# Kernel optimization log

Measured on AMD Instinct MI355X. Metric: run time of the kernel, lower is better.

Reference implementation:

```python
import jax, jax.numpy as jnp
import numpy as np

D_MODEL = 1024
D_STATE = 16
D_CONV = 4
EXPAND = 2
D_INNER = EXPAND * D_MODEL          # 2048
DT_RANK = (D_MODEL + 15) // 16      # 64
B, L = 4, 2048


def setup_inputs() -> dict:
    key = jax.random.key(0)
    ks = jax.random.split(key, 10)
    s = 0.02
    x = jax.random.normal(ks[0], (B, L, D_MODEL), dtype=jnp.float32)
    # weights stored (in, out) so y = x @ W
    W_in = jax.random.normal(ks[1], (D_MODEL, 2 * D_INNER), dtype=jnp.float32) * s
    conv_w = jax.random.normal(ks[2], (D_INNER, D_CONV), dtype=jnp.float32) * 0.2
    conv_b = jnp.zeros((D_INNER,), dtype=jnp.float32)
    W_xproj = jax.random.normal(ks[3], (D_INNER, DT_RANK + 2 * D_STATE), dtype=jnp.float32) * s
    W_dt = jax.random.normal(ks[4], (DT_RANK, D_INNER), dtype=jnp.float32) * s
    b_dt = jax.random.uniform(ks[5], (D_INNER,), dtype=jnp.float32, minval=-4.0, maxval=-2.0)
    # S4D real init: A = -exp(A_log), A_log = log(1..d_state)
    A_log = jnp.log(jnp.broadcast_to(jnp.arange(1, D_STATE + 1, dtype=jnp.float32), (D_INNER, D_STATE)))
    Dp = jnp.ones((D_INNER,), dtype=jnp.float32)
    W_out = jax.random.normal(ks[6], (D_INNER, D_MODEL), dtype=jnp.float32) * s
    return {"x": x, "W_in": W_in, "conv_w": conv_w, "conv_b": conv_b,
            "W_xproj": W_xproj, "W_dt": W_dt, "b_dt": b_dt,
            "A_log": A_log, "Dp": Dp, "W_out": W_out}


def _causal_depthwise_conv(u, conv_w, conv_b):
    # u: (B, L, D_INNER); depthwise causal conv, kernel D_CONV
    uc = jnp.transpose(u, (0, 2, 1))                      # (B, D, L)
    k = conv_w[:, None, :]                                # (D, 1, K)
    y = jax.lax.conv_general_dilated(
        uc, k, window_strides=(1,), padding=[(D_CONV - 1, 0)],
        feature_group_count=D_INNER,
        dimension_numbers=('NCH', 'OIH', 'NCH'))
    y = y + conv_b[None, :, None]
    return jnp.transpose(y, (0, 2, 1))                    # (B, L, D)


def _selective_scan(u, delta, A, Bm, Cm, Dp):
    # u, delta: (B, L, d); A: (d, n); Bm, Cm: (B, L, n)
    def step(h, inp):
        u_t, dt_t, B_t, C_t = inp                         # (B,d),(B,d),(B,n),(B,n)
        dA = jnp.exp(dt_t[..., None] * A)                 # (B, d, n)
        h = h * dA + (dt_t * u_t)[..., None] * B_t[:, None, :]
        y = jnp.einsum('bdn,bn->bd', h, C_t)
        return h, y

    h0 = jnp.zeros((u.shape[0], u.shape[2], A.shape[1]), dtype=u.dtype)
    xs = (jnp.swapaxes(u, 0, 1), jnp.swapaxes(delta, 0, 1),
          jnp.swapaxes(Bm, 0, 1), jnp.swapaxes(Cm, 0, 1))
    _, ys = jax.lax.scan(step, h0, xs)
    y = jnp.swapaxes(ys, 0, 1)                            # (B, L, d)
    return y + u * Dp


def reference(x, W_in, conv_w, conv_b, W_xproj, W_dt, b_dt, A_log, Dp, W_out):
    xz = x @ W_in                                         # (B, L, 2*D_INNER)
    u, z = jnp.split(xz, 2, axis=-1)
    u = jax.nn.silu(_causal_depthwise_conv(u, conv_w, conv_b))
    proj = u @ W_xproj                                    # (B, L, DT_RANK + 2*D_STATE)
    dt_r = proj[..., :DT_RANK]
    Bm = proj[..., DT_RANK:DT_RANK + D_STATE]
    Cm = proj[..., DT_RANK + D_STATE:]
    delta = jax.nn.softplus(dt_r @ W_dt + b_dt)           # (B, L, D_INNER)
    A = -jnp.exp(A_log)                                   # (D_INNER, D_STATE)
    y = _selective_scan(u, delta, A, Bm, Cm, Dp)
    y = y * jax.nn.silu(z)
    return y @ W_out
```

## Files before the change

### kernel.cpp

```cpp
#include <hip/hip_runtime.h>
#include <hip/hip_bf16.h>
#include <math.h>

#define MTOK   8192
#define LSEQ   2048
#define NBATCH 4
#define DMODEL 1024
#define DINNER 2048
#define DSTATE 16
#define DTRANK 64
#define NXZ    4096
#define CHUNK  64
#define NCH    32
#define NPROJ  (MTOK * 96)
#define SPLITK 8

typedef _Float16 f16;
using f16x8 = __attribute__((ext_vector_type(8))) _Float16;
using f16x4 = __attribute__((ext_vector_type(4))) _Float16;
using f32x4 = __attribute__((ext_vector_type(4))) float;

__device__ __forceinline__ float silu_f(float x) { return x / (1.f + __expf(-x)); }

__device__ __forceinline__ void gload_lds16(const void* g, void* l) {
    __builtin_amdgcn_global_load_lds(
        (const __attribute__((address_space(1))) void*)g,
        (__attribute__((address_space(3))) void*)l, 16, 0, 0);
}

__global__ __launch_bounds__(256)
void cvt_f2h(const float* __restrict__ in, f16* __restrict__ out, int n4)
{
    const int i = blockIdx.x * 256 + threadIdx.x;
    if (i >= n4) return;
    const float4 v = ((const float4*)in)[i];
    f16x4 o;
    o[0] = (f16)v.x; o[1] = (f16)v.y; o[2] = (f16)v.z; o[3] = (f16)v.w;
    ((f16x4*)out)[i] = o;
}

__global__ __launch_bounds__(256)
void tcvt(const float* __restrict__ in, f16* __restrict__ out, int R, int C)
{
    __shared__ float t[32][33];
    const int c0 = blockIdx.x * 32, r0 = blockIdx.y * 32;
    const int tx = threadIdx.x & 31, ty = threadIdx.x >> 5;
    #pragma unroll
    for (int j = 0; j < 4; ++j)
        t[ty + 8 * j][tx] = in[(size_t)(r0 + ty + 8 * j) * C + c0 + tx];
    __syncthreads();
    #pragma unroll
    for (int j = 0; j < 4; ++j)
        out[(size_t)(c0 + ty + 8 * j) * R + r0 + tx] = (f16)t[tx][ty + 8 * j];
}

template<int EPI, int SWZ, typename OUT_T>
__global__ __launch_bounds__(256)
void hgemm128(const f16* __restrict__ A, int lda,
              const f16* __restrict__ Bt, int ldb,
              OUT_T* __restrict__ C, int ldc,
              int K, const float* __restrict__ bias,
              OUT_T* __restrict__ C2, int splitcol)
{
    __shared__ __align__(16) f16 As[2][128 * 32];
    __shared__ __align__(16) f16 Bs[2][128 * 32];

    int bx = blockIdx.x, by = blockIdx.y;
    if (SWZ) {
        const int gx = gridDim.x;
        const int nwg = gx * gridDim.y;
        const int lin = by * gx + bx;
        const int q = nwg >> 3;
        const int swz = (lin & 7) * q + (lin >> 3);
        bx = swz % gx; by = swz / gx;
    }

    const int tid  = threadIdx.x;
    const int lane = tid & 63, wave = tid >> 6;
    const int wr = wave >> 1, wc = wave & 1;
    const int row0 = bx * 128;
    int col0 = by * 128;

    const int lrow = lane >> 2, lcol = (lane & 3) * 8;
    const f16* Agw = A  + (size_t)(row0 + wave * 32 + lrow) * lda + lcol;
    const f16* Bgw = Bt + (size_t)(col0 + wave * 32 + lrow) * ldb + lcol;
    const int ldsbase = (wave * 32) * 32;

    const int frow = lane & 15, fk = (lane >> 4) * 8;
    const int nt = K / 32;

    f32x4 acc[4][4] = {};

    #pragma unroll
    for (int r = 0; r < 2; ++r) {
        gload_lds16(Agw + (size_t)r * 16 * lda, &As[0][ldsbase + r * 16 * 32]);
        gload_lds16(Bgw + (size_t)r * 16 * ldb, &Bs[0][ldsbase + r * 16 * 32]);
    }

    int cur = 0;
    for (int kt = 0; kt < nt; ++kt) {
        __syncthreads();
        if (kt + 1 < nt) {
            const int k0 = (kt + 1) * 32;
            #pragma unroll
            for (int r = 0; r < 2; ++r) {
                gload_lds16(Agw + (size_t)r * 16 * lda + k0, &As[cur ^ 1][ldsbase + r * 16 * 32]);
                gload_lds16(Bgw + (size_t)r * 16 * ldb + k0, &Bs[cur ^ 1][ldsbase + r * 16 * 32]);
            }
        }
        f16x8 af[4], bf[4];
        #pragma unroll
        for (int m = 0; m < 4; ++m)
            af[m] = *(const f16x8*)&As[cur][(wr * 64 + m * 16 + frow) * 32 + fk];
        #pragma unroll
        for (int n = 0; n < 4; ++n)
            bf[n] = *(const f16x8*)&Bs[cur][(wc * 64 + n * 16 + frow) * 32 + fk];
        #pragma unroll
        for (int m = 0; m < 4; ++m)
            #pragma unroll
            for (int n = 0; n < 4; ++n)
                acc[m][n] = __builtin_amdgcn_mfma_f32_16x16x32_f16(af[m], bf[n], acc[m][n], 0, 0, 0);
        cur ^= 1;
    }

    OUT_T* Cw = C;
    if (C2 != nullptr && col0 >= splitcol) { Cw = C2; col0 -= splitcol; }

    const int rbase = row0 + wr * 64 + (lane >> 4) * 4;
    const int cbase = col0 + wc * 64 + (lane & 15);
    #pragma unroll
    for (int m = 0; m < 4; ++m) {
        #pragma unroll
        for (int n = 0; n < 4; ++n) {
            const int col = cbase + n * 16;
            #pragma unroll
            for (int r = 0; r < 4; ++r) {
                const int row = rbase + m * 16 + r;
                float tv = acc[m][n][r];
                if (EPI == 1) {
                    tv += bias[col];
                    tv = (tv > 20.f) ? tv : __logf(1.f + __expf(tv));
                }
                Cw[(size_t)row * ldc + col] = (OUT_T)tv;
            }
        }
    }
}

__global__ __launch_bounds__(256)
void hgemm_n96(const f16* __restrict__ A,
               const f16* __restrict__ Bt,
               float* __restrict__ part)
{
    __shared__ __align__(16) f16 As[128][40];
    __shared__ __align__(16) f16 Bs[96][40];

    const int tid = threadIdx.x, lane = tid & 63, wave = tid >> 6;
    const int row0 = blockIdx.x * 128;
    const int sk = blockIdx.y;
    const int kbase = sk * (DINNER / SPLITK);

    const int srow = tid >> 1, skoff = (tid & 1) * 16;
    const f16* Ag = A  + (size_t)(row0 + srow) * DINNER + kbase + skoff;
    const f16* Bg = Bt + (size_t)srow * DINNER + kbase + skoff;

    const int frow = lane & 15, fk = (lane >> 4) * 8;

    f32x4 acc[2][6] = {};

    for (int kk = 0; kk < DINNER / SPLITK; kk += 32) {
        const f16x8 a0 = *(const f16x8*)(Ag + kk);
        const f16x8 a1 = *(const f16x8*)(Ag + kk + 8);
        f16x8 b0 = {}, b1 = {};
        if (tid < 192) { b0 = *(const f16x8*)(Bg + kk); b1 = *(const f16x8*)(Bg + kk + 8); }
        __syncthreads();
        *(f16x8*)&As[srow][skoff]     = a0;
        *(f16x8*)&As[srow][skoff + 8] = a1;
        if (tid < 192) {
            *(f16x8*)&Bs[srow][skoff]     = b0;
            *(f16x8*)&Bs[srow][skoff + 8] = b1;
        }
        __syncthreads();

        f16x8 af[2], bf[6];
        #pragma unroll
        for (int m = 0; m < 2; ++m)
            af[m] = *(const f16x8*)&As[wave * 32 + m * 16 + frow][fk];
        #pragma unroll
        for (int n = 0; n < 6; ++n)
            bf[n] = *(const f16x8*)&Bs[n * 16 + frow][fk];
        #pragma unroll
        for (int m = 0; m < 2; ++m)
            #pragma unroll
            for (int n = 0; n < 6; ++n)
                acc[m][n] = __builtin_amdgcn_mfma_f32_16x16x32_f16(af[m], bf[n], acc[m][n], 0, 0, 0);
    }

    #pragma unroll
    for (int m = 0; m < 2; ++m)
        #pragma unroll
        for (int n = 0; n < 6; ++n) {
            const int col = n * 16 + (lane & 15);
            #pragma unroll
            for (int r = 0; r < 4; ++r) {
                const int row = row0 + wave * 32 + m * 16 + (lane >> 4) * 4 + r;
                part[((size_t)sk * MTOK + row) * 96 + col] = acc[m][n][r];
            }
        }
}

__global__ __launch_bounds__(256)
void reduce3(const float* __restrict__ part, float* __restrict__ proj,
             f16* __restrict__ projh)
{
    const int e = blockIdx.x * 256 + threadIdx.x;
    float s = 0.f;
    #pragma unroll
    for (int i = 0; i < SPLITK; ++i) s += part[(size_t)i * NPROJ + e];
    proj[e]  = s;
    projh[e] = (f16)s;
}

__global__ __launch_bounds__(256)
void conv_silu_kernel(const f16* __restrict__ uph,
                      const float* __restrict__ cw, const float* __restrict__ cb,
                      f16* __restrict__ uh)
{
    const int mt  = blockIdx.x;
    const int ml0 = mt * 8;
    const int l0  = ml0 & (LSEQ - 1);
    const int d   = threadIdx.x * 8;

    float w[8][4];
    #pragma unroll
    for (int c = 0; c < 8; ++c) {
        const float4 wv = *(const float4*)(cw + (size_t)(d + c) * 4);
        w[c][0] = wv.x; w[c][1] = wv.y; w[c][2] = wv.z; w[c][3] = wv.w;
    }
    float bias[8];
    {
        const float4 b0 = *(const float4*)(cb + d);
        const float4 b1 = *(const float4*)(cb + d + 4);
        bias[0] = b0.x; bias[1] = b0.y; bias[2] = b0.z; bias[3] = b0.w;
        bias[4] = b1.x; bias[5] = b1.y; bias[6] = b1.z; bias[7] = b1.w;
    }

    f16x8 r[11];
    if (l0 != 0) {
        #pragma unroll
        for (int i = 0; i < 11; ++i)
            r[i] = *(const f16x8*)(uph + (size_t)(ml0 - 3 + i) * DINNER + d);
    } else {
        r[0] = f16x8{}; r[1] = f16x8{}; r[2] = f16x8{};
        #pragma unroll
        for (int i = 3; i < 11; ++i)
            r[i] = *(const f16x8*)(uph + (size_t)(ml0 - 3 + i) * DINNER + d);
    }

    #pragma unroll
    for (int i = 0; i < 8; ++i) {
        f16x8 o;
        #pragma unroll
        for (int c = 0; c < 8; ++c) {
            float a = bias[c];
            #pragma unroll
            for (int j = 0; j < 4; ++j)
                a = fmaf((float)r[i + j][c], w[c][j], a);
            o[c] = (f16)silu_f(a);
        }
        *(f16x8*)(uh + (size_t)(ml0 + i) * DINNER + d) = o;
    }
}

__device__ __forceinline__ bool load_A(const float* __restrict__ A_log, int d,
                                       float* Av)
{
    #pragma unroll
    for (int n = 0; n < DSTATE; ++n)
        Av[n] = -__expf(A_log[(size_t)d * DSTATE + n]);
    bool p = true;
    #pragma unroll
    for (int n = 1; n < DSTATE; ++n) {
        const float r = Av[n] / Av[0];
        if (fabsf(r - (float)(n + 1)) > 1e-3f) p = false;
    }
    return p;
}

__global__ __launch_bounds__(256)
void scan_pass1(const f16* __restrict__ uh,
                const f16* __restrict__ deltah,
                const float* __restrict__ proj,
                const float* __restrict__ A_log,
                float* __restrict__ Sbuf, float* __restrict__ sumdt)
{
    const int d = blockIdx.x * 256 + threadIdx.x;
    const int c = blockIdx.y;
    const int b = blockIdx.z;

    float Av[DSTATE];
    const bool pw = load_A(A_log, d, Av);
    const float Av0 = Av[0];

    const float* projb = proj + ((size_t)b * LSEQ + (size_t)c * CHUNK) * 96 + 64;

    float S[DSTATE];
    #pragma unroll
    for (int n = 0; n < DSTATE; ++n) S[n] = 0.f;
    float sdt = 0.f;

    const size_t tok0 = (size_t)b * LSEQ + (size_t)c * CHUNK;
    if (pw) {
        for (int l = 0; l < CHUNK; ++l) {
            const float* pr = projb + (size_t)l * 96;
            const float dt = (float)deltah[(tok0 + l) * DINNER + d];
            const float uu = (float)uh[(tok0 + l) * DINNER + d];
            sdt += dt;
            const float du = dt * uu;
            const float p1 = __expf(dt * Av0);
            const float p2 = p1 * p1;
            const float p3 = p2 * p1;
            const float p4 = p2 * p2;
            float m = 1.f;
            #pragma unroll
            for (int g = 0; g < 4; ++g) {
                const f32x4 bb = *(const f32x4*)(pr + g * 4);
                S[g*4+0] = fmaf(S[g*4+0], m * p1, du * bb[0]);
                S[g*4+1] = fmaf(S[g*4+1], m * p2, du * bb[1]);
                S[g*4+2] = fmaf(S[g*4+2], m * p3, du * bb[2]);
                S[g*4+3] = fmaf(S[g*4+3], m * p4, du * bb[3]);
                m *= p4;
            }
        }
    } else {
        for (int l = 0; l < CHUNK; ++l) {
            const float* pr = projb + (size_t)l * 96;
            const float dt = (float)deltah[(tok0 + l) * DINNER + d];
            const float uu = (float)uh[(tok0 + l) * DINNER + d];
            sdt += dt;
            const float du = dt * uu;
            #pragma unroll
            for (int n = 0; n < DSTATE; ++n)
                S[n] = fmaf(S[n], __expf(dt * Av[n]), du * pr[n]);
        }
    }

    const size_t base = (size_t)b * NCH + c;
    #pragma unroll
    for (int n = 0; n < DSTATE; ++n)
        Sbuf[(base * DSTATE + n) * DINNER + d] = S[n];
    sumdt[base * DINNER + d] = sdt;
}

__global__ __launch_bounds__(256)
void scan_pass2(const float* __restrict__ A_log,
                const float* __restrict__ sumdt,
                float* __restrict__ Sbuf)
{
    const int d = blockIdx.x * 256 + threadIdx.x;
    const int b = blockIdx.y;

    float Av[DSTATE];
    const bool pw = load_A(A_log, d, Av);
    const float Av0 = Av[0];

    float h[DSTATE];
    #pragma unroll
    for (int n = 0; n < DSTATE; ++n) h[n] = 0.f;

    for (int c = 0; c < NCH; ++c) {
        const size_t base = (size_t)b * NCH + c;
        const float sdt = sumdt[base * DINNER + d];
        if (pw) {
            const float p1 = __expf(sdt * Av0);
            const float p2 = p1 * p1;
            const float p3 = p2 * p1;
            const float p4 = p2 * p2;
            float m = 1.f;
            #pragma unroll
            for (int g = 0; g < 4; ++g) {
                const float pj[4] = {p1, p2, p3, p4};
                #pragma unroll
                for (int j = 0; j < 4; ++j) {
                    const int n = g * 4 + j;
                    const size_t idx = (base * DSTATE + n) * DINNER + d;
                    const float tmp = Sbuf[idx];
                    Sbuf[idx] = h[n];
                    h[n] = fmaf(h[n], m * pj[j], tmp);
                }
                m *= p4;
            }
        } else {
            #pragma unroll
            for (int n = 0; n < DSTATE; ++n) {
                const size_t idx = (base * DSTATE + n) * DINNER + d;
                const float tmp = Sbuf[idx];
                Sbuf[idx] = h[n];
                h[n] = fmaf(h[n], __expf(sdt * Av[n]), tmp);
            }
        }
    }
}

__global__ __launch_bounds__(256)
void scan_pass3(const f16* __restrict__ uh,
                const f16* __restrict__ deltah,
                const f16* __restrict__ zh,
                const float* __restrict__ proj,
                const float* __restrict__ A_log,
                const float* __restrict__ Dp,
                const float* __restrict__ Sbuf,
                f16* __restrict__ ygh)
{
    const int d = blockIdx.x * 256 + threadIdx.x;
    const int c = blockIdx.y;
    const int b = blockIdx.z;

    float Av[DSTATE];
    const bool pw = load_A(A_log, d, Av);
    const float Av0 = Av[0];

    float h[DSTATE];
    const size_t base = (size_t)b * NCH + c;
    #pragma unroll
    for (int n = 0; n < DSTATE; ++n)
        h[n] = Sbuf[(base * DSTATE + n) * DINNER + d];

    const float Dval = Dp[d];
    const float* projb = proj + ((size_t)b * LSEQ + (size_t)c * CHUNK) * 96 + 64;

    const size_t tok0 = (size_t)b * LSEQ + (size_t)c * CHUNK;
    for (int l = 0; l < CHUNK; ++l) {
        const float* pr = projb + (size_t)l * 96;
        const size_t tok = tok0 + l;
        const float dt = (float)deltah[tok * DINNER + d];
        const float uu = (float)uh[tok * DINNER + d];
        const float zz = (float)zh[tok * DINNER + d];
        const float du = dt * uu;
        float y = 0.f;
        if (pw) {
            const float p1 = __expf(dt * Av0);
            const float p2 = p1 * p1;
            const float p3 = p2 * p1;
            const float p4 = p2 * p2;
            float m = 1.f;
            #pragma unroll
            for (int g = 0; g < 4; ++g) {
                const f32x4 bb = *(const f32x4*)(pr + g * 4);
                const f32x4 cc = *(const f32x4*)(pr + 16 + g * 4);
                h[g*4+0] = fmaf(h[g*4+0], m * p1, du * bb[0]);
                h[g*4+1] = fmaf(h[g*4+1], m * p2, du * bb[1]);
                h[g*4+2] = fmaf(h[g*4+2], m * p3, du * bb[2]);
                h[g*4+3] = fmaf(h[g*4+3], m * p4, du * bb[3]);
                y = fmaf(h[g*4+0], cc[0], y);
                y = fmaf(h[g*4+1], cc[1], y);
                y = fmaf(h[g*4+2], cc[2], y);
                y = fmaf(h[g*4+3], cc[3], y);
                m *= p4;
            }
        } else {
            #pragma unroll
            for (int n = 0; n < DSTATE; ++n) {
                h[n] = fmaf(h[n], __expf(dt * Av[n]), du * pr[n]);
                y = fmaf(h[n], pr[16 + n], y);
            }
        }
        const float yt = fmaf(uu, Dval, y);
        ygh[tok * DINNER + d] = (f16)(yt * silu_f(zz));
    }
}

extern "C" void kernel_launch(void* const* d_in, const int* in_sizes, int n_in,
                              void* d_out, int out_size, void* d_ws, size_t ws_size,
                              hipStream_t stream)
{
    const float* x     = (const float*)d_in[0];
    const float* W_in  = (const float*)d_in[1];
    const float* cw    = (const float*)d_in[2];
    const float* cb    = (const float*)d_in[3];
    const float* W_xp  = (const float*)d_in[4];
    const float* W_dt  = (const float*)d_in[5];
    const float* b_dt  = (const float*)d_in[6];
    const float* A_log = (const float*)d_in[7];
    const float* Dp    = (const float*)d_in[8];
    const float* W_out = (const float*)d_in[9];
    float* out = (float*)d_out;

    float* updelta = (float*)d_ws;
    f16*   zh      = (f16*)(updelta + (size_t)MTOK * DINNER);
    f16*   uh      = zh + (size_t)MTOK * DINNER;
    float* proj    = (float*)(uh + (size_t)MTOK * DINNER);
    f16*   projh   = (f16*)(proj + NPROJ);
    float* Sbuf    = (float*)(projh + NPROJ);
    float* sumdt   = Sbuf + (size_t)NBATCH * NCH * DSTATE * DINNER;
    f16*   WxpT    = (f16*)(sumdt + (size_t)NBATCH * NCH * DINNER);
    f16*   WdtT    = WxpT + (size_t)96 * DINNER;
    f16*   WoutT   = WdtT + (size_t)DINNER * DTRANK;
    f16*   big     = WoutT + (size_t)DMODEL * DINNER;
    f16*   WinT    = big;
    float* part3   = (float*)(big + (size_t)NXZ * DMODEL);
    f16*   ygh     = big;
    f16*   xh      = uh;
    f16*   uph     = (f16*)updelta;
    f16*   deltah  = (f16*)updelta;

    cvt_f2h<<<(MTOK * DMODEL / 4 + 255) / 256, 256, 0, stream>>>(x, xh, MTOK * DMODEL / 4);
    tcvt<<<dim3(NXZ / 32, DMODEL / 32), 256, 0, stream>>>(W_in, WinT, DMODEL, NXZ);

    hgemm128<0, 1, f16><<<dim3(64, 32), 256, 0, stream>>>(
        xh, DMODEL, WinT, DMODEL, uph, DINNER, DMODEL, nullptr, zh, DINNER);

    conv_silu_kernel<<<MTOK / 8, 256, 0, stream>>>(uph, cw, cb, uh);

    tcvt<<<dim3(96 / 32, DINNER / 32), 256, 0, stream>>>(W_xp, WxpT, DINNER, 96);
    hgemm_n96<<<dim3(64, SPLITK), 256, 0, stream>>>(uh, WxpT, part3);
    reduce3<<<NPROJ / 256, 256, 0, stream>>>(part3, proj, projh);

    tcvt<<<dim3(DINNER / 32, DTRANK / 32), 256, 0, stream>>>(W_dt, WdtT, DTRANK, DINNER);
    hgemm128<1, 0, f16><<<dim3(64, 16), 256, 0, stream>>>(
        projh, 96, WdtT, DTRANK, deltah, DINNER, DTRANK, b_dt, nullptr, 0);

    scan_pass1<<<dim3(DINNER / 256, NCH, NBATCH), 256, 0, stream>>>(
        uh, deltah, proj, A_log, Sbuf, sumdt);
    scan_pass2<<<dim3(DINNER / 256, NBATCH), 256, 0, stream>>>(A_log, sumdt, Sbuf);
    scan_pass3<<<dim3(DINNER / 256, NCH, NBATCH), 256, 0, stream>>>(
        uh, deltah, zh, proj, A_log, Dp, Sbuf, ygh);

    tcvt<<<dim3(DMODEL / 32, DINNER / 32), 256, 0, stream>>>(W_out, WoutT, DINNER, DMODEL);
    hgemm128<0, 1, float><<<dim3(64, 8), 256, 0, stream>>>(
        ygh, DINNER, WoutT, DINNER, out, DMODEL, DINNER, nullptr, nullptr, 0);
}
```

Before: 344.4 us.

## Use k-chunk-major LDS layout in hgemm128 and drop block swizzle

The GEMM's shared-memory tiles move from a row-major 128x32 layout to a k-chunk-major layout: four 8-element k groups, each holding 128 rows. Global-to-LDS loads are remapped so that each thread writes contiguous 16-byte chunks, and the MFMA fragment reads now stride by 16 bytes per row. The aim is to remove LDS bank conflicts on the fragment reads. The workgroup index swizzle used for L2 locality is also removed, which may hurt cache reuse on the large GEMMs.

```diff
diff --git a/kernel.cpp b/kernel.cpp
--- a/kernel.cpp
+++ b/kernel.cpp
@@ -54,7 +54,7 @@
         out[(size_t)(c0 + ty + 8 * j) * R + r0 + tx] = (f16)t[tx][ty + 8 * j];
 }
 
-template<int EPI, int SWZ, typename OUT_T>
+template<int EPI, typename OUT_T>
 __global__ __launch_bounds__(256)
 void hgemm128(const f16* __restrict__ A, int lda,
               const f16* __restrict__ Bt, int ldb,
@@ -62,59 +62,47 @@
               int K, const float* __restrict__ bias,
               OUT_T* __restrict__ C2, int splitcol)
 {
-    __shared__ __align__(16) f16 As[2][128 * 32];
-    __shared__ __align__(16) f16 Bs[2][128 * 32];
-
-    int bx = blockIdx.x, by = blockIdx.y;
-    if (SWZ) {
-        const int gx = gridDim.x;
-        const int nwg = gx * gridDim.y;
-        const int lin = by * gx + bx;
-        const int q = nwg >> 3;
-        const int swz = (lin & 7) * q + (lin >> 3);
-        bx = swz % gx; by = swz / gx;
-    }
+    __shared__ __align__(16) f16 As[2][512 * 8];
+    __shared__ __align__(16) f16 Bs[2][512 * 8];
 
     const int tid  = threadIdx.x;
     const int lane = tid & 63, wave = tid >> 6;
     const int wr = wave >> 1, wc = wave & 1;
-    const int row0 = bx * 128;
-    int col0 = by * 128;
-
-    const int lrow = lane >> 2, lcol = (lane & 3) * 8;
-    const f16* Agw = A  + (size_t)(row0 + wave * 32 + lrow) * lda + lcol;
-    const f16* Bgw = Bt + (size_t)(col0 + wave * 32 + lrow) * ldb + lcol;
-    const int ldsbase = (wave * 32) * 32;
-
-    const int frow = lane & 15, fk = (lane >> 4) * 8;
+    const int row0 = blockIdx.x * 128;
+    int col0 = blockIdx.y * 128;
+
+    const int ch0 = tid,        kcb0 = ch0 >> 7, crow0 = ch0 & 127;
+    const int ch1 = 256 + tid,  kcb1 = ch1 >> 7, crow1 = ch1 & 127;
+    const f16* A0 = A  + (size_t)(row0 + crow0) * lda + kcb0 * 8;
+    const f16* A1 = A  + (size_t)(row0 + crow1) * lda + kcb1 * 8;
+    const f16* B0 = Bt + (size_t)(col0 + crow0) * ldb + kcb0 * 8;
+    const f16* B1 = Bt + (size_t)(col0 + crow1) * ldb + kcb1 * 8;
+
+    const int frow = lane & 15, g16 = lane >> 4;
     const int nt = K / 32;
 
     f32x4 acc[4][4] = {};
 
-    #pragma unroll
-    for (int r = 0; r < 2; ++r) {
-        gload_lds16(Agw + (size_t)r * 16 * lda, &As[0][ldsbase + r * 16 * 32]);
-        gload_lds16(Bgw + (size_t)r * 16 * ldb, &Bs[0][ldsbase + r * 16 * 32]);
-    }
+    auto stage = [&](int buf, int k0) {
+        gload_lds16(A0 + k0, &As[buf][(size_t)ch0 * 8]);
+        gload_lds16(A1 + k0, &As[buf][(size_t)ch1 * 8]);
+        gload_lds16(B0 + k0, &Bs[buf][(size_t)ch0 * 8]);
+        gload_lds16(B1 + k0, &Bs[buf][(size_t)ch1 * 8]);
+    };
+
+    stage(0, 0);
 
     int cur = 0;
     for (int kt = 0; kt < nt; ++kt) {
         __syncthreads();
-        if (kt + 1 < nt) {
-            const int k0 = (kt + 1) * 32;
-            #pragma unroll
-            for (int r = 0; r < 2; ++r) {
-                gload_lds16(Agw + (size_t)r * 16 * lda + k0, &As[cur ^ 1][ldsbase + r * 16 * 32]);
-                gload_lds16(Bgw + (size_t)r * 16 * ldb + k0, &Bs[cur ^ 1][ldsbase + r * 16 * 32]);
-            }
-        }
+        if (kt + 1 < nt) stage(cur ^ 1, (kt + 1) * 32);
         f16x8 af[4], bf[4];
         #pragma unroll
         for (int m = 0; m < 4; ++m)
-            af[m] = *(const f16x8*)&As[cur][(wr * 64 + m * 16 + frow) * 32 + fk];
+            af[m] = *(const f16x8*)&As[cur][(size_t)(g16 * 128 + wr * 64 + m * 16 + frow) * 8];
         #pragma unroll
         for (int n = 0; n < 4; ++n)
-            bf[n] = *(const f16x8*)&Bs[cur][(wc * 64 + n * 16 + frow) * 32 + fk];
+            bf[n] = *(const f16x8*)&Bs[cur][(size_t)(g16 * 128 + wc * 64 + n * 16 + frow) * 8];
         #pragma unroll
         for (int m = 0; m < 4; ++m)
             #pragma unroll
@@ -507,7 +495,7 @@
     cvt_f2h<<<(MTOK * DMODEL / 4 + 255) / 256, 256, 0, stream>>>(x, xh, MTOK * DMODEL / 4);
     tcvt<<<dim3(NXZ / 32, DMODEL / 32), 256, 0, stream>>>(W_in, WinT, DMODEL, NXZ);
 
-    hgemm128<0, 1, f16><<<dim3(64, 32), 256, 0, stream>>>(
+    hgemm128<0, f16><<<dim3(64, 32), 256, 0, stream>>>(
         xh, DMODEL, WinT, DMODEL, uph, DINNER, DMODEL, nullptr, zh, DINNER);
 
     conv_silu_kernel<<<MTOK / 8, 256, 0, stream>>>(uph, cw, cb, uh);
@@ -517,7 +505,7 @@
     reduce3<<<NPROJ / 256, 256, 0, stream>>>(part3, proj, projh);
 
     tcvt<<<dim3(DINNER / 32, DTRANK / 32), 256, 0, stream>>>(W_dt, WdtT, DTRANK, DINNER);
-    hgemm128<1, 0, f16><<<dim3(64, 16), 256, 0, stream>>>(
+    hgemm128<1, f16><<<dim3(64, 16), 256, 0, stream>>>(
         projh, 96, WdtT, DTRANK, deltah, DINNER, DTRANK, b_dt, nullptr, 0);
 
     scan_pass1<<<dim3(DINNER / 256, NCH, NBATCH), 256, 0, stream>>>(
@@ -527,6 +515,6 @@
         uh, deltah, zh, proj, A_log, Dp, Sbuf, ygh);
 
     tcvt<<<dim3(DMODEL / 32, DINNER / 32), 256, 0, stream>>>(W_out, WoutT, DINNER, DMODEL);
-    hgemm128<0, 1, float><<<dim3(64, 8), 256, 0, stream>>>(
+    hgemm128<0, float><<<dim3(64, 8), 256, 0, stream>>>(
         ygh, DINNER, WoutT, DINNER, out, DMODEL, DINNER, nullptr, nullptr, 0);
 }
```

Measured after the change: 392.9 us. 1.14x slower.
